# Kernel tuning notes

Hardware: AMD Instinct MI355X
Metric: run time of the kernel (lower is better)

Reference implementation:

```python
import jax, jax.numpy as jnp
import numpy as np

N_ENT = 100000
N_REL = 200
D_IN = 128
D_HID = 128
D_OUT = 128
N_BASES = 50
N_EDGES = 800000
N_TRIPLES = 4096
BN_EPS = 1e-5


def setup_inputs() -> dict:
    key = jax.random.key(0)
    ks = jax.random.split(key, 16)
    xavier = lambda k, shape: jax.random.normal(k, shape, jnp.float32) * np.sqrt(2.0 / (shape[-2] + shape[-1]))
    inp = {
        'entity_embeds': xavier(ks[0], (N_ENT, D_IN)),
        'bases': xavier(ks[1], (N_BASES, D_IN)),
        'coefficients': xavier(ks[2], (N_REL, N_BASES)),
        'self_rel_embed': xavier(ks[3], (1, D_IN)),
        'W1': xavier(ks[4], (3, D_IN, D_HID)),
        'relw1': xavier(ks[5], (D_IN, D_HID)),
        'bn1_gamma': jnp.ones((D_HID,), jnp.float32),
        'bn1_beta': jnp.zeros((D_HID,), jnp.float32),
        'W2': xavier(ks[6], (3, D_HID, D_OUT)),
        'relw2': xavier(ks[7], (D_HID, D_OUT)),
        'bn2_gamma': jnp.ones((D_OUT,), jnp.float32),
        'bn2_beta': jnp.zeros((D_OUT,), jnp.float32),
        'ent_ids': jnp.arange(N_ENT, dtype=jnp.int32),
        'edge_index': jax.random.randint(ks[8], (2, N_EDGES), 0, N_ENT, jnp.int32),
        'edge_type': jax.random.randint(ks[9], (N_EDGES,), 0, 2 * N_REL + 1, jnp.int32),
        'y': jax.random.randint(ks[10], (N_EDGES,), 0, 3, jnp.int32),
    }
    heads = jax.random.randint(ks[11], (N_TRIPLES,), 0, N_ENT, jnp.int32)
    rels = jax.random.randint(ks[12], (N_TRIPLES,), 0, 2 * N_REL + 1, jnp.int32)
    tails = jax.random.randint(ks[13], (N_TRIPLES,), 0, N_ENT, jnp.int32)
    inp['triples'] = jnp.stack([heads, rels, tails], axis=1)
    return inp


def _compgcn_layer(x, r, edge_index, edge_type, y, W, relw, gamma, beta):
    src, dst = edge_index[0], edge_index[1]
    # message: gather neighbor & relation embeds, edge-direction-conditioned matmul
    msgs = x[src] - r[edge_type]                      # [E, d_in]
    out = jnp.zeros((msgs.shape[0], W.shape[-1]), msgs.dtype)
    for k in range(3):  # y in {0,1,2}: masked matmul instead of [E,d,d] gather
        mask = (y == k)[:, None]
        out = out + jnp.where(mask, msgs, 0.0) @ W[k]
    # scatter-add aggregation at destination nodes
    agg = jax.ops.segment_sum(out, dst, num_segments=x.shape[0])  # [N, d_out]
    # BatchNorm1d (training-mode batch statistics, biased var)
    mean = jnp.mean(agg, axis=0)
    var = jnp.mean(jnp.square(agg - mean), axis=0)
    bn = (agg - mean) * jax.lax.rsqrt(var + BN_EPS) * gamma + beta
    return jnp.tanh(bn), r @ relw


def reference(entity_embeds, bases, coefficients, self_rel_embed, W1, relw1,
              bn1_gamma, bn1_beta, W2, relw2, bn2_gamma, bn2_beta,
              ent_ids, edge_index, edge_type, y, triples):
    x = entity_embeds[ent_ids]
    r = coefficients @ bases                           # basis-composed relations
    r = jnp.concatenate([r, -r, self_rel_embed], axis=0)  # [2R+1, d]
    x, r = _compgcn_layer(x, r, edge_index, edge_type, y, W1, relw1, bn1_gamma, bn1_beta)
    x, r = _compgcn_layer(x, r, edge_index, edge_type, y, W2, relw2, bn2_gamma, bn2_beta)
    # decode: TransE-style L1 score
    h = x[triples[:, 0]]
    re = r[triples[:, 1]]
    t = x[triples[:, 2]]
    scores = jnp.sum(jnp.abs(h + re - t), axis=1)      # p=1 norm
    return scores
```

## Files before the change

### kernel.cpp

```cpp
#include <hip/hip_runtime.h>
#include <cstdint>

typedef __attribute__((ext_vector_type(8))) short short8;
typedef __attribute__((ext_vector_type(4))) float f32x4;

static __device__ __forceinline__ unsigned short f2bf(float f) {
  unsigned int u = __float_as_uint(f);
  unsigned int r = (u + 0x7FFFu + ((u >> 16) & 1u)) >> 16;
  return (unsigned short)r;
}
static __device__ __forceinline__ unsigned int pack2bf(float a, float b) {
  return (unsigned int)f2bf(a) | ((unsigned int)f2bf(b) << 16);
}
static __device__ __forceinline__ float2 bf2f(unsigned int u) {
  return make_float2(__uint_as_float(u << 16), __uint_as_float(u & 0xFFFF0000u));
}
static __device__ __forceinline__ void acc8(float* a, uint4 h, uint4 r) {
  float2 f, g;
  f = bf2f(h.x); g = bf2f(r.x); a[0] += f.x - g.x; a[1] += f.y - g.y;
  f = bf2f(h.y); g = bf2f(r.y); a[2] += f.x - g.x; a[3] += f.y - g.y;
  f = bf2f(h.z); g = bf2f(r.z); a[4] += f.x - g.x; a[5] += f.y - g.y;
  f = bf2f(h.w); g = bf2f(r.w); a[6] += f.x - g.x; a[7] += f.y - g.y;
}

__global__ __launch_bounds__(256) void k_prep(
    const float* __restrict__ coeff, const float* __restrict__ bases,
    const float* __restrict__ selfr, const float* __restrict__ relw1,
    const float* __restrict__ relw2,
    unsigned int* __restrict__ rfb, unsigned int* __restrict__ r1b,
    float* __restrict__ r2,
    const float* __restrict__ W1, const float* __restrict__ W2,
    unsigned short* __restrict__ WT1, unsigned short* __restrict__ WT2,
    const float* __restrict__ ent, const int* __restrict__ ent_ids,
    unsigned int* __restrict__ entbf,
    int* __restrict__ counts, float* __restrict__ stats,
    int nPairs, int nKeys, int cvtB, int cntB) {
  int b = blockIdx.x, tid = threadIdx.x;
  if (b < 201) {
    __shared__ float row[2][128], r1row[2][128];
    int half = tid >> 7, c = tid & 127;
    int r = 2 * b + half;
    bool ok = (r <= 400);
    if (ok) {
      float v;
      if (r == 400) {
        v = selfr[c];
      } else {
        int rr = (r < 200) ? r : r - 200;
        float s = 0.f;
#pragma unroll 10
        for (int k = 0; k < 50; ++k) s += coeff[rr * 50 + k] * bases[k * 128 + c];
        v = (r < 200) ? s : -s;
      }
      row[half][c] = v;
    }
    __syncthreads();
    if (ok && c < 64) rfb[r * 64 + c] = pack2bf(row[half][2 * c], row[half][2 * c + 1]);
    if (ok) {
      float s = 0.f;
#pragma unroll 8
      for (int k = 0; k < 128; ++k) s += row[half][k] * relw1[k * 128 + c];
      r1row[half][c] = s;
    }
    __syncthreads();
    if (ok && c < 64) r1b[r * 64 + c] = pack2bf(r1row[half][2 * c], r1row[half][2 * c + 1]);
    if (ok) {
      float s = 0.f;
#pragma unroll 8
      for (int k = 0; k < 128; ++k) s += r1row[half][k] * relw2[k * 128 + c];
      r2[r * 128 + c] = s;
    }
  } else if (b < 585) {
    int idx = (b - 201) * 256 + tid;
    const int half = 128 * 384;
    const float* W = (idx < half) ? W1 : W2;
    unsigned short* WT = (idx < half) ? WT1 : WT2;
    int id2 = (idx < half) ? idx : idx - half;
    int n = id2 & 127, k = id2 >> 7;
    int kk = k >> 7, kr = k & 127;
    WT[(size_t)n * 384 + k] = f2bf(W[(size_t)kk * 16384 + kr * 128 + n]);
  } else if (b < 585 + cvtB) {
    int i = (b - 585) * 256 + tid;
    if (i < nPairs) {
      int e = i >> 6;
      int src = ent_ids[e];
      float2 v = *(const float2*)&ent[(size_t)src * 128 + (i & 63) * 2];
      entbf[i] = pack2bf(v.x, v.y);
    }
  } else if (b < 585 + cvtB + cntB) {
    int i = (b - (585 + cvtB)) * 256 + tid;
    if (i < nKeys) counts[i] = 0;
  } else {
    int i = (b - (585 + cvtB + cntB)) * 256 + tid;
    if (i < 16896) stats[i] = 0.f;
  }
}

__global__ __launch_bounds__(256) void k_histR(const int* __restrict__ ei, const int* __restrict__ y,
                                               int* __restrict__ counts, int nE, int rsz) {
  int r = blockIdx.x;
  int e0 = blockIdx.y * 1024;
#pragma unroll
  for (int i = 0; i < 4; ++i) {
    int e = e0 + i * 256 + threadIdx.x;
    if (e < nE) {
      int key = ei[nE + e] * 3 + y[e];
      if (key / rsz == r) atomicAdd(&counts[key], 1);
    }
  }
}

__global__ void k_scan1(const int* __restrict__ counts, int* __restrict__ local,
                        int* __restrict__ blockSums, int n) {
  __shared__ int sdata[1024];
  int tid = threadIdx.x;
  int i = blockIdx.x * 1024 + tid;
  int v = (i < n) ? counts[i] : 0;
  sdata[tid] = v;
  __syncthreads();
  for (int off = 1; off < 1024; off <<= 1) {
    int t = (tid >= off) ? sdata[tid - off] : 0;
    __syncthreads();
    sdata[tid] += t;
    __syncthreads();
  }
  if (i < n) local[i] = sdata[tid] - v;
  if (tid == 1023) blockSums[blockIdx.x] = sdata[1023];
}

__global__ void k_scan2(const int* __restrict__ blockSums, int* __restrict__ carries,
                        int* __restrict__ offsets, int n, int nb) {
  __shared__ int sdata[1024];
  int tid = threadIdx.x;
  int v = (tid < nb) ? blockSums[tid] : 0;
  sdata[tid] = v;
  __syncthreads();
  for (int off = 1; off < 1024; off <<= 1) {
    int t = (tid >= off) ? sdata[tid - off] : 0;
    __syncthreads();
    sdata[tid] += t;
    __syncthreads();
  }
  if (tid < nb) carries[tid] = sdata[tid] - v;
  if (tid == 1023) offsets[n] = sdata[1023];
}

__global__ void k_scan3(const int* __restrict__ local, const int* __restrict__ carries,
                        int* __restrict__ offsets, int* __restrict__ cursor, int n) {
  int i = blockIdx.x * 1024 + threadIdx.x;
  if (i >= n) return;
  int v = local[i] + carries[blockIdx.x];
  offsets[i] = v;
  cursor[i] = v;
}

__global__ __launch_bounds__(256) void k_fillR(const int* __restrict__ ei, const int* __restrict__ et,
                                               const int* __restrict__ y, int* __restrict__ cursor,
                                               unsigned int* __restrict__ bucket, int nE, int rsz) {
  int r = blockIdx.x;
  int e0 = blockIdx.y * 1024;
#pragma unroll
  for (int i = 0; i < 4; ++i) {
    int e = e0 + i * 256 + threadIdx.x;
    if (e < nE) {
      int key = ei[nE + e] * 3 + y[e];
      if (key / rsz == r) {
        int slot = atomicAdd(&cursor[key], 1);
        bucket[slot] = (unsigned int)ei[e] | ((unsigned int)et[e] << 20);
      }
    }
  }
}

__global__ __launch_bounds__(256, 6) void k_fused(
    const unsigned int* __restrict__ xb, const unsigned int* __restrict__ rb,
    const int* __restrict__ offsets, const unsigned int* __restrict__ packed,
    const unsigned short* __restrict__ WT, unsigned short* __restrict__ C,
    float* __restrict__ statsRep, int M) {
  __shared__ unsigned short As[32][392];
  __shared__ float sSum[128], sSq[128];
  const int tid = threadIdx.x;
  const int m0 = blockIdx.x * 32;
  const int wave = tid >> 6, lane = tid & 63;
  const int quad = lane >> 4, l16 = lane & 15;
  const int qid = (wave << 2) | quad;
  if (tid < 128) { sSum[tid] = 0.f; sSq[tid] = 0.f; }

  {
    const int dst0 = m0 + 2 * qid;
    int b0, b1, b2, b3, b4, b5, b6;
    if (dst0 + 1 < M) {
      const int base = dst0 * 3;
      b0 = offsets[base];     b1 = offsets[base + 1];
      b2 = offsets[base + 2]; b3 = offsets[base + 3];
      b4 = offsets[base + 4]; b5 = offsets[base + 5];
      b6 = offsets[base + 6];
    } else if (dst0 < M) {
      const int base = dst0 * 3;
      b0 = offsets[base];     b1 = offsets[base + 1];
      b2 = offsets[base + 2]; b3 = offsets[base + 3];
      b4 = b3; b5 = b3; b6 = b3;
    } else {
      b0 = b1 = b2 = b3 = b4 = b5 = b6 = 0;
    }
    float ac[8] = {};
    int seg = 0;
    int nextB = b1;
    int j = b0;
    const int hi = b6;
    unsigned short* lds0 = &As[2 * qid][0];

    auto flushSeg = [&]() {
      int rowOff = (seg >= 3) ? 392 : 0;
      int cls = seg - ((seg >= 3) ? 3 : 0);
      uint4 ov;
      ov.x = pack2bf(ac[0], ac[1]);
      ov.y = pack2bf(ac[2], ac[3]);
      ov.z = pack2bf(ac[4], ac[5]);
      ov.w = pack2bf(ac[6], ac[7]);
      *(uint4*)(lds0 + rowOff + cls * 128 + l16 * 8) = ov;
#pragma unroll
      for (int z = 0; z < 8; ++z) ac[z] = 0.f;
      ++seg;
      nextB = (seg == 1) ? b2 : (seg == 2) ? b3 : (seg == 3) ? b4
            : (seg == 4) ? b5 : b6;
    };

    if (j < hi) {
      int jc1 = (j + 1 < hi) ? j + 1 : j;
      unsigned int q0 = packed[j], q1 = packed[jc1];
      int s0 = q0 & 0xFFFFF, t0 = q0 >> 20;
      int s1 = q1 & 0xFFFFF, t1 = q1 >> 20;
      uint4 h0 = *(const uint4*)&xb[(size_t)s0 * 64 + l16 * 4];
      uint4 r0 = *(const uint4*)&rb[(size_t)t0 * 64 + l16 * 4];
      uint4 h1 = *(const uint4*)&xb[(size_t)s1 * 64 + l16 * 4];
      uint4 r1 = *(const uint4*)&rb[(size_t)t1 * 64 + l16 * 4];
      while (j < hi) {
        int jp2 = (j + 2 < hi) ? j + 2 : hi - 1;
        int jp3 = (j + 3 < hi) ? j + 3 : hi - 1;
        unsigned int q2 = packed[jp2], q3 = packed[jp3];
        int s2 = q2 & 0xFFFFF, t2 = q2 >> 20;
        int s3 = q3 & 0xFFFFF, t3 = q3 >> 20;
        uint4 th0 = *(const uint4*)&xb[(size_t)s2 * 64 + l16 * 4];
        uint4 tr0 = *(const uint4*)&rb[(size_t)t2 * 64 + l16 * 4];
        uint4 th1 = *(const uint4*)&xb[(size_t)s3 * 64 + l16 * 4];
        uint4 tr1 = *(const uint4*)&rb[(size_t)t3 * 64 + l16 * 4];
        while (j == nextB) flushSeg();
        acc8(ac, h0, r0);
        ++j;
        if (j < hi) {
          while (j == nextB) flushSeg();
          acc8(ac, h1, r1);
          ++j;
        }
        h0 = th0; r0 = tr0; h1 = th1; r1 = tr1;
      }
    }
    while (seg < 6) flushSeg();
  }
  __syncthreads();

  const unsigned short* Wp = WT + (size_t)(wave * 32 + l16) * 384 + quad * 8;
  short8 bc0 = *(const short8*)(Wp);
  short8 bc1 = *(const short8*)(Wp + 16 * 384);
  f32x4 acc[2][2] = {};
#pragma unroll 1
  for (int it = 0; it < 12; ++it) {
    short8 bn0, bn1;
    if (it < 11) {
      bn0 = *(const short8*)(Wp + (it + 1) * 32);
      bn1 = *(const short8*)(Wp + 16 * 384 + (it + 1) * 32);
    }
    short8 a0 = *(const short8*)&As[l16][it * 32 + quad * 8];
    short8 a1 = *(const short8*)&As[16 + l16][it * 32 + quad * 8];
    acc[0][0] = __builtin_amdgcn_mfma_f32_16x16x32_bf16(a0, bc0, acc[0][0], 0, 0, 0);
    acc[0][1] = __builtin_amdgcn_mfma_f32_16x16x32_bf16(a0, bc1, acc[0][1], 0, 0, 0);
    acc[1][0] = __builtin_amdgcn_mfma_f32_16x16x32_bf16(a1, bc0, acc[1][0], 0, 0, 0);
    acc[1][1] = __builtin_amdgcn_mfma_f32_16x16x32_bf16(a1, bc1, acc[1][1], 0, 0, 0);
    if (it < 11) { bc0 = bn0; bc1 = bn1; }
  }

  float ps[2] = {}, pq[2] = {};
#pragma unroll
  for (int t = 0; t < 2; ++t)
#pragma unroll
    for (int reg = 0; reg < 4; ++reg) {
      int m = m0 + t * 16 + quad * 4 + reg;
      if (m < M) {
#pragma unroll
        for (int ct = 0; ct < 2; ++ct) {
          float v = acc[t][ct][reg];
          int col = wave * 32 + ct * 16 + l16;
          C[(size_t)m * 128 + col] = f2bf(v);
          ps[ct] += v; pq[ct] += v * v;
        }
      }
    }
#pragma unroll
  for (int ct = 0; ct < 2; ++ct) {
    int col = wave * 32 + ct * 16 + l16;
    atomicAdd(&sSum[col], ps[ct]);
    atomicAdd(&sSq[col], pq[ct]);
  }
  __syncthreads();
  if (tid < 128) {
    float* rep = statsRep + ((blockIdx.x & 31) << 8);
    atomicAdd(&rep[tid], sSum[tid]);
    atomicAdd(&rep[128 + tid], sSq[tid]);
  }
}

__global__ void k_norm(const uint4* __restrict__ Cb4, const float* __restrict__ rep,
                       const float* __restrict__ gamma, const float* __restrict__ beta,
                       float invN, uint4* __restrict__ xb4, int nQuad) {
  __shared__ float sc_s[128], bi_s[128];
  if (threadIdx.x < 128) {
    int c = threadIdx.x;
    float s = 0.f, q = 0.f;
#pragma unroll
    for (int r = 0; r < 32; ++r) {
      s += rep[r * 256 + c];
      q += rep[r * 256 + 128 + c];
    }
    float mean = s * invN;
    float var = fmaxf(q * invN - mean * mean, 0.f);
    float sc = rsqrtf(var + 1e-5f) * gamma[c];
    sc_s[c] = sc;
    bi_s[c] = beta[c] - mean * sc;
  }
  __syncthreads();
  int i = blockIdx.x * blockDim.x + threadIdx.x;
  if (i >= nQuad) return;
  uint4 v = Cb4[i];
  int j = (i * 4) & 63;
  uint4 o;
  float2 f;
  f = bf2f(v.x);
  o.x = pack2bf(tanhf(fmaf(f.x, sc_s[2*j],   bi_s[2*j])),   tanhf(fmaf(f.y, sc_s[2*j+1], bi_s[2*j+1])));
  f = bf2f(v.y);
  o.y = pack2bf(tanhf(fmaf(f.x, sc_s[2*j+2], bi_s[2*j+2])), tanhf(fmaf(f.y, sc_s[2*j+3], bi_s[2*j+3])));
  f = bf2f(v.z);
  o.z = pack2bf(tanhf(fmaf(f.x, sc_s[2*j+4], bi_s[2*j+4])), tanhf(fmaf(f.y, sc_s[2*j+5], bi_s[2*j+5])));
  f = bf2f(v.w);
  o.w = pack2bf(tanhf(fmaf(f.x, sc_s[2*j+6], bi_s[2*j+6])), tanhf(fmaf(f.y, sc_s[2*j+7], bi_s[2*j+7])));
  xb4[i] = o;
}

__global__ void k_score(const unsigned int* __restrict__ xb, const float* __restrict__ r,
                        const int* __restrict__ triples, float* __restrict__ out, int nT) {
  int gid = blockIdx.x * blockDim.x + threadIdx.x;
  int t = gid >> 6;
  if (t >= nT) return;
  int lane = gid & 63;
  int h = triples[t * 3], rel = triples[t * 3 + 1], tl = triples[t * 3 + 2];
  float2 a = bf2f(xb[(size_t)h * 64 + lane]);
  float2 b = *(const float2*)&r[(size_t)rel * 128 + lane * 2];
  float2 cc = bf2f(xb[(size_t)tl * 64 + lane]);
  float s = fabsf(a.x + b.x - cc.x) + fabsf(a.y + b.y - cc.y);
#pragma unroll
  for (int off = 32; off > 0; off >>= 1) s += __shfl_down(s, off);
  if (lane == 0) out[t] = s;
}

extern "C" void kernel_launch(void* const* d_in, const int* in_sizes, int n_in,
                              void* d_out, int out_size, void* d_ws, size_t ws_size,
                              hipStream_t stream) {
  const float* ent   = (const float*)d_in[0];
  const float* bases = (const float*)d_in[1];
  const float* coeff = (const float*)d_in[2];
  const float* selfr = (const float*)d_in[3];
  const float* W1    = (const float*)d_in[4];
  const float* relw1 = (const float*)d_in[5];
  const float* g1    = (const float*)d_in[6];
  const float* b1    = (const float*)d_in[7];
  const float* W2    = (const float*)d_in[8];
  const float* relw2 = (const float*)d_in[9];
  const float* g2    = (const float*)d_in[10];
  const float* b2    = (const float*)d_in[11];
  const int* ent_ids = (const int*)d_in[12];
  const int* ei      = (const int*)d_in[13];
  const int* et      = (const int*)d_in[14];
  const int* yk      = (const int*)d_in[15];
  const int* triples = (const int*)d_in[16];

  const int M  = in_sizes[0] / 128;
  const int nE = in_sizes[14];
  const int nT = in_sizes[16] / 3;
  const int nKeys = M * 3;
  const int nScanBlocks = (nKeys + 1023) / 1024;
  const int rsz = (nKeys + 7) / 8;

  float* p = (float*)d_ws;
  float* r2    = p; p += 401 * 128;
  float* statsAll = p; p += 16896;
  float* rep1 = statsAll;
  float* rep2 = statsAll + 32 * 256;
  unsigned short* Cb  = (unsigned short*)p;
  unsigned int* entbf = (unsigned int*)(Cb + (size_t)M * 128);
  unsigned int* xb    = entbf + (size_t)M * 64;
  unsigned int* rfb   = xb + (size_t)M * 64;
  unsigned int* r1b   = rfb + 401 * 64;
  unsigned short* WT1 = (unsigned short*)(r1b + 401 * 64);
  unsigned short* WT2 = WT1 + 128 * 384;
  int* counts  = (int*)(WT2 + 128 * 384);
  int* offsets = counts + nKeys;
  int* cursor  = offsets + nKeys + 1;
  int* slocal  = cursor + nKeys;
  int* sblock  = slocal + nKeys;
  int* scarry  = sblock + nScanBlocks;
  unsigned int* bucket = (unsigned int*)(scarry + nScanBlocks);

  float* out = (float*)d_out;

  const int nPairs = M * 64;
  const int nQuad  = M * 16;
  const int cvtB = (nPairs + 255) / 256;
  const int cntB = (nKeys + 255) / 256;
  const int zeroB = 66;
  const int prepBlocks = 585 + cvtB + cntB + zeroB;
  const int fusedBlocks = (M + 31) / 32;
  const int normBlocks = (nQuad + 255) / 256;
  const dim3 rangedGrid(8, (nE + 1023) / 1024);

  k_prep<<<prepBlocks, 256, 0, stream>>>(coeff, bases, selfr, relw1, relw2,
                                         rfb, r1b, r2, W1, W2, WT1, WT2,
                                         ent, ent_ids, entbf, counts, statsAll,
                                         nPairs, nKeys, cvtB, cntB);

  k_histR<<<rangedGrid, 256, 0, stream>>>(ei, yk, counts, nE, rsz);
  k_scan1<<<nScanBlocks, 1024, 0, stream>>>(counts, slocal, sblock, nKeys);
  k_scan2<<<1, 1024, 0, stream>>>(sblock, scarry, offsets, nKeys, nScanBlocks);
  k_scan3<<<nScanBlocks, 1024, 0, stream>>>(slocal, scarry, offsets, cursor, nKeys);
  k_fillR<<<rangedGrid, 256, 0, stream>>>(ei, et, yk, cursor, bucket, nE, rsz);

  k_fused<<<fusedBlocks, 256, 0, stream>>>(entbf, rfb, offsets, bucket, WT1,
                                           Cb, rep1, M);
  k_norm<<<normBlocks, 256, 0, stream>>>((const uint4*)Cb, rep1, g1, b1,
                                         1.0f / M, (uint4*)xb, nQuad);

  k_fused<<<fusedBlocks, 256, 0, stream>>>(xb, r1b, offsets, bucket, WT2,
                                           Cb, rep2, M);
  k_norm<<<normBlocks, 256, 0, stream>>>((const uint4*)Cb, rep2, g2, b2,
                                         1.0f / M, (uint4*)xb, nQuad);

  k_score<<<(nT * 64 + 255) / 256, 256, 0, stream>>>(xb, r2, triples, out, nT);
}
```

Baseline: 399.5 us.

## Replace range-partitioned histogram/fill with single-pass atomics; shuffle-reduce BN stats

The histogram and bucket-fill kernels previously ran 8 passes over all edges, each handling only keys in one range to keep atomics localized. They now do a single pass with global atomics over all keys, which cuts edge reads by a factor of 8 at the cost of scattered atomics across the whole counts array. The fused kernel's BatchNorm statistics reduction also drops the shared-memory atomics and the block barrier. It uses cross-quad wave shuffles instead, with direct global atomics from one quad per wave.

```diff
diff --git a/kernel.cpp b/kernel.cpp
--- a/kernel.cpp
+++ b/kernel.cpp
@@ -96,16 +96,25 @@
   }
 }
 
-__global__ __launch_bounds__(256) void k_histR(const int* __restrict__ ei, const int* __restrict__ y,
-                                               int* __restrict__ counts, int nE, int rsz) {
-  int r = blockIdx.x;
-  int e0 = blockIdx.y * 1024;
-#pragma unroll
-  for (int i = 0; i < 4; ++i) {
-    int e = e0 + i * 256 + threadIdx.x;
+__global__ __launch_bounds__(256) void k_hist(const int* __restrict__ ei, const int* __restrict__ y,
+                                              int* __restrict__ counts, int nE) {
+  int e = blockIdx.x * 1024 + threadIdx.x;
+#pragma unroll
+  for (int i = 0; i < 4; ++i, e += 256) {
+    if (e < nE) atomicAdd(&counts[ei[nE + e] * 3 + y[e]], 1);
+  }
+}
+
+__global__ __launch_bounds__(256) void k_fill(const int* __restrict__ ei, const int* __restrict__ et,
+                                              const int* __restrict__ y, int* __restrict__ cursor,
+                                              unsigned int* __restrict__ bucket, int nE) {
+  int e = blockIdx.x * 1024 + threadIdx.x;
+#pragma unroll
+  for (int i = 0; i < 4; ++i, e += 256) {
     if (e < nE) {
       int key = ei[nE + e] * 3 + y[e];
-      if (key / rsz == r) atomicAdd(&counts[key], 1);
+      int slot = atomicAdd(&cursor[key], 1);
+      bucket[slot] = (unsigned int)ei[e] | ((unsigned int)et[e] << 20);
     }
   }
 }
@@ -154,37 +163,17 @@
   cursor[i] = v;
 }
 
-__global__ __launch_bounds__(256) void k_fillR(const int* __restrict__ ei, const int* __restrict__ et,
-                                               const int* __restrict__ y, int* __restrict__ cursor,
-                                               unsigned int* __restrict__ bucket, int nE, int rsz) {
-  int r = blockIdx.x;
-  int e0 = blockIdx.y * 1024;
-#pragma unroll
-  for (int i = 0; i < 4; ++i) {
-    int e = e0 + i * 256 + threadIdx.x;
-    if (e < nE) {
-      int key = ei[nE + e] * 3 + y[e];
-      if (key / rsz == r) {
-        int slot = atomicAdd(&cursor[key], 1);
-        bucket[slot] = (unsigned int)ei[e] | ((unsigned int)et[e] << 20);
-      }
-    }
-  }
-}
-
 __global__ __launch_bounds__(256, 6) void k_fused(
     const unsigned int* __restrict__ xb, const unsigned int* __restrict__ rb,
     const int* __restrict__ offsets, const unsigned int* __restrict__ packed,
     const unsigned short* __restrict__ WT, unsigned short* __restrict__ C,
     float* __restrict__ statsRep, int M) {
   __shared__ unsigned short As[32][392];
-  __shared__ float sSum[128], sSq[128];
   const int tid = threadIdx.x;
   const int m0 = blockIdx.x * 32;
   const int wave = tid >> 6, lane = tid & 63;
   const int quad = lane >> 4, l16 = lane & 15;
   const int qid = (wave << 2) | quad;
-  if (tid < 128) { sSum[tid] = 0.f; sSq[tid] = 0.f; }
 
   {
     const int dst0 = m0 + 2 * qid;
@@ -298,15 +287,19 @@
     }
 #pragma unroll
   for (int ct = 0; ct < 2; ++ct) {
-    int col = wave * 32 + ct * 16 + l16;
-    atomicAdd(&sSum[col], ps[ct]);
-    atomicAdd(&sSq[col], pq[ct]);
-  }
-  __syncthreads();
-  if (tid < 128) {
+    ps[ct] += __shfl_xor(ps[ct], 16);
+    ps[ct] += __shfl_xor(ps[ct], 32);
+    pq[ct] += __shfl_xor(pq[ct], 16);
+    pq[ct] += __shfl_xor(pq[ct], 32);
+  }
+  if (quad == 0) {
     float* rep = statsRep + ((blockIdx.x & 31) << 8);
-    atomicAdd(&rep[tid], sSum[tid]);
-    atomicAdd(&rep[128 + tid], sSq[tid]);
+#pragma unroll
+    for (int ct = 0; ct < 2; ++ct) {
+      int col = wave * 32 + ct * 16 + l16;
+      atomicAdd(&rep[col], ps[ct]);
+      atomicAdd(&rep[128 + col], pq[ct]);
+    }
   }
 }
 
@@ -388,7 +381,6 @@
   const int nT = in_sizes[16] / 3;
   const int nKeys = M * 3;
   const int nScanBlocks = (nKeys + 1023) / 1024;
-  const int rsz = (nKeys + 7) / 8;
 
   float* p = (float*)d_ws;
   float* r2    = p; p += 401 * 128;
@@ -420,18 +412,18 @@
   const int prepBlocks = 585 + cvtB + cntB + zeroB;
   const int fusedBlocks = (M + 31) / 32;
   const int normBlocks = (nQuad + 255) / 256;
-  const dim3 rangedGrid(8, (nE + 1023) / 1024);
+  const int edgeBlocks = (nE + 1023) / 1024;
 
   k_prep<<<prepBlocks, 256, 0, stream>>>(coeff, bases, selfr, relw1, relw2,
                                          rfb, r1b, r2, W1, W2, WT1, WT2,
                                          ent, ent_ids, entbf, counts, statsAll,
                                          nPairs, nKeys, cvtB, cntB);
 
-  k_histR<<<rangedGrid, 256, 0, stream>>>(ei, yk, counts, nE, rsz);
+  k_hist<<<edgeBlocks, 256, 0, stream>>>(ei, yk, counts, nE);
   k_scan1<<<nScanBlocks, 1024, 0, stream>>>(counts, slocal, sblock, nKeys);
   k_scan2<<<1, 1024, 0, stream>>>(sblock, scarry, offsets, nKeys, nScanBlocks);
   k_scan3<<<nScanBlocks, 1024, 0, stream>>>(slocal, scarry, offsets, cursor, nKeys);
-  k_fillR<<<rangedGrid, 256, 0, stream>>>(ei, et, yk, cursor, bucket, nE, rsz);
+  k_fill<<<edgeBlocks, 256, 0, stream>>>(ei, et, yk, cursor, bucket, nE);
 
   k_fused<<<fusedBlocks, 256, 0, stream>>>(entbf, rfb, offsets, bucket, WT1,
                                            Cb, rep1, M);
```

New measurement: 402.5 us. Within noise of the previous version (+0.8%).
